# Kernel optimization log

Hardware: AMD Instinct MI355X
Metric: run time of the kernel (lower is better)

Reference implementation:

```python
import jax, jax.numpy as jnp
import numpy as np

B, N, DIM, HEADS, DH = 2, 2048, 512, 8, 64
DIM_INNER = HEADS * DH
SCALE = DH ** -0.5


def setup_inputs() -> dict:
    key = jax.random.key(0)
    ks = jax.random.split(key, 8)
    w = lambda k: jax.random.normal(k, (DIM, DIM_INNER), dtype=jnp.float32) * 0.02
    return {
        'x': jax.random.normal(ks[0], (B, N, DIM), dtype=jnp.float32),
        'w_q_u': w(ks[1]), 'w_k_u': w(ks[2]), 'w_v_u': w(ks[3]),
        'w_q_c': w(ks[4]), 'w_k_c': w(ks[5]), 'w_v_c': w(ks[6]),
        'w_out': jax.random.normal(ks[7], (DIM_INNER, DIM), dtype=jnp.float32) * 0.02,
    }


def _split_heads(t):
    b, n, _ = t.shape
    return t.reshape(b, n, HEADS, DH).transpose(0, 2, 1, 3)  # b h n d


def reference(x, w_q_u, w_k_u, w_v_u, w_q_c, w_k_c, w_v_c, w_out):
    b, n, _ = x.shape
    Qu, Ku, Vu = (_split_heads(x @ w) for w in (w_q_u, w_k_u, w_v_u))
    Qc, Kc, Vc = (_split_heads(x @ w) for w in (w_q_c, w_k_c, w_v_c))

    i = jnp.arange(n)[:, None]
    j = jnp.arange(n)[None, :]
    neg_inf = jnp.float32(-jnp.inf)
    causal_mask = jnp.where(j > i, neg_inf, 0.0)      # -inf strictly above diag
    lookahead_mask = jnp.where(j <= i, neg_inf, 0.0)  # -inf on/below diag
    binary_causal = (j <= i).astype(x.dtype)          # lower-tri ones incl diag

    term1 = jnp.einsum('bhid,bhjd->bhij', Qc, Vu) * SCALE * binary_causal
    sigmoid_term = jax.nn.sigmoid(jnp.einsum('bhid,bhjd->bhij', Qu, Ku) * SCALE + lookahead_mask)
    S_u = jnp.einsum('bhij,bhkj->bhik', term1, sigmoid_term)
    S_c = jnp.einsum('bhid,bhjd->bhij', Qc, Kc) * SCALE + causal_mask

    final_scores = S_c - jax.nn.silu(S_u)
    attn = jax.nn.softmax(final_scores, axis=-1)
    out = jnp.einsum('bhij,bhjd->bhid', attn, Vc)
    out = out.transpose(0, 2, 1, 3).reshape(b, n, DIM_INNER)  # merge heads
    return out @ w_out
```

## Files before the change

kernel.cpp:

```cpp
#include <hip/hip_runtime.h>
#include <hip/hip_bf16.h>

typedef _Float16 h16;
typedef _Float16 h16x8 __attribute__((ext_vector_type(8)));
typedef float f32x4 __attribute__((ext_vector_type(4)));

#define DEVI static __device__ __forceinline__

constexpr int NN = 2048;
constexpr int DIM = 512;
constexpr int NH = 8;
constexpr int DH = 64;
constexpr int BH = 16;
constexpr float FSCALE = 0.125f;

DEVI f32x4 mfma16(h16x8 a, h16x8 b, f32x4 c) {
  return __builtin_amdgcn_mfma_f32_16x16x32_f16(a, b, c, 0, 0, 0);
}

DEVI void glds16(const void* g, void* l) {
  __builtin_amdgcn_global_load_lds(
      (const __attribute__((address_space(1))) unsigned int*)g,
      (__attribute__((address_space(3))) unsigned int*)l, 16, 0, 0);
}

DEVI void tri_decode(int p, int& a, int& b) {
  a = (int)((sqrtf(8.f * p + 1.f) - 1.f) * 0.5f);
  while ((a + 1) * (a + 2) / 2 <= p) ++a;
  while (a * (a + 1) / 2 > p) --a;
  b = p - a * (a + 1) / 2;
}


__global__ __launch_bounds__(256) void k_pack_x(const float* __restrict__ x, h16* __restrict__ xh) {
  int i = (blockIdx.x * 256 + threadIdx.x) * 4;
  float4 v = *(const float4*)(x + i);
  union { h16 h[4]; uint2 u; } pk;
  pk.h[0] = (h16)v.x; pk.h[1] = (h16)v.y; pk.h[2] = (h16)v.z; pk.h[3] = (h16)v.w;
  *(uint2*)(xh + i) = pk.u;
}

struct WPtrs { const float* w[7]; };

__global__ __launch_bounds__(256) void k_pack_w(WPtrs wp, h16* __restrict__ wt) {
  const float* W = wp.w[blockIdx.z];
  h16* out = wt + (size_t)blockIdx.z * DIM * DIM;
  __shared__ h16 t[64][65];
  int k0 = blockIdx.x * 64, o0 = blockIdx.y * 64;
  int c = threadIdx.x & 63, r4 = threadIdx.x >> 6;
#pragma unroll
  for (int rr = 0; rr < 64; rr += 4) {
    int r = rr + r4;
    t[r][c] = (h16)W[(size_t)(k0 + r) * DIM + o0 + c];
  }
  __syncthreads();
#pragma unroll
  for (int rr = 0; rr < 64; rr += 4) {
    int r = rr + r4;
    out[(size_t)(o0 + r) * DIM + k0 + c] = t[c][r];
  }
}

__global__ __launch_bounds__(256) void k_proj(const h16* __restrict__ xh, const h16* __restrict__ wt,
                                              h16* __restrict__ qkv, h16* __restrict__ vcT) {
  __shared__ h16 pool[128 * 136];
  h16* Al = pool;
  h16* Bl = pool + 128 * 64;
  int m0 = blockIdx.x * 128, o0 = blockIdx.y * 128;
  int lane = threadIdx.x & 63, wv = threadIdx.x >> 6;
  int wy = wv >> 1, wx = wv & 1;
  int srow = 32 * wv;
  int lr = lane >> 3, lc = 8 * (lane & 7);
  f32x4 acc[4][4] = {};
  for (int ks0 = 0; ks0 < DIM; ks0 += 64) {
#pragma unroll
    for (int inst = 0; inst < 4; inst++) {
      int r = srow + 8 * inst;
      glds16(xh + (size_t)(m0 + r + lr) * DIM + ks0 + lc, Al + r * 64);
      glds16(wt + (size_t)(o0 + r + lr) * DIM + ks0 + lc, Bl + r * 64);
    }
    __syncthreads();
#pragma unroll
    for (int ks = 0; ks < 2; ks++) {
      h16x8 af[4], bfv[4];
      int co = 32 * ks + 8 * (lane >> 4);
#pragma unroll
      for (int i = 0; i < 4; i++) af[i] = *(const h16x8*)(Al + (64 * wy + 16 * i + (lane & 15)) * 64 + co);
#pragma unroll
      for (int j = 0; j < 4; j++) bfv[j] = *(const h16x8*)(Bl + (64 * wx + 16 * j + (lane & 15)) * 64 + co);
#pragma unroll
      for (int i = 0; i < 4; i++)
#pragma unroll
        for (int j = 0; j < 4; j++) acc[i][j] = mfma16(af[i], bfv[j], acc[i][j]);
    }
    __syncthreads();
  }
  int widx = o0 >> 9;
  float scl = (widx == 0 || widx == 3) ? FSCALE : 1.0f;
  h16 (*Clds)[136] = (h16(*)[136])pool;
#pragma unroll
  for (int i = 0; i < 4; i++)
#pragma unroll
    for (int j = 0; j < 4; j++)
#pragma unroll
      for (int r = 0; r < 4; r++) {
        int rloc = 64 * wy + 16 * i + (lane >> 4) * 4 + r;
        int cloc = 64 * wx + 16 * j + (lane & 15);
        Clds[rloc][cloc] = (h16)(acc[i][j][r] * scl);
      }
  __syncthreads();
  int t = threadIdx.x;
  {
    int rloc = t >> 1, half = t & 1;
    int gi = m0 + rloc;
    int b = gi >> 11, n = gi & 2047;
    int og = o0 + 64 * half;
    int h = (og >> 6) & 7;
    h16* dst = qkv + (((size_t)widx * BH + b * NH + h) * NN + n) * DH;
#pragma unroll
    for (int e = 0; e < 8; e++)
      *(h16x8*)(dst + 8 * e) = *(const h16x8*)&Clds[rloc][64 * half + 8 * e];
  }
  if (widx == 5) {
    int c = t & 127, rq = t >> 7;
    int og = o0 + c;
    int h = (og >> 6) & 7, d = og & 63;
    int b = m0 >> 11, nb = (m0 & 2047) + rq * 64;
    h16* dst = vcT + ((size_t)(b * NH + h) * DH + d) * NN + nb;
#pragma unroll
    for (int g = 0; g < 8; g++) {
      h16x8 w;
#pragma unroll
      for (int e = 0; e < 8; e++) w[e] = Clds[rq * 64 + 8 * g + e][c];
      *(h16x8*)(dst + 8 * g) = w;
    }
  }
}

__global__ __launch_bounds__(256) void k_termsig(const h16* __restrict__ qkv,
                                                 h16* __restrict__ term, h16* __restrict__ sig, int bh0) {
  int pidx = blockIdx.x;
  int lz = blockIdx.z, bh = bh0 + lz;
  int a, bq;
  tri_decode(pidx, a, bq);
  int lane = threadIdx.x & 63, wv = threadIdx.x >> 6;
  int wy = wv >> 1, wx = wv & 1;
  int l15 = lane & 15, q4 = lane >> 4;
  int lr = lane >> 3, lchunk = lane & 7;
  __shared__ h16 pool[128 * 136];
  h16* Al = pool;
  h16* Bl = pool + 128 * 64;
  size_t slot = ((size_t)lz * 136 + (size_t)a * (a + 1) / 2 + bq) * 16384;

  for (int ph = 0; ph < 2; ph++) {
    bool is_sig = (ph == 1);
    int rt = is_sig ? bq : a;
    int jt = is_sig ? a : bq;
    const h16* A  = qkv + ((size_t)(is_sig ? 0 : 3) * BH + bh) * NN * DH;
    const h16* Bv = qkv + ((size_t)(is_sig ? 1 : 2) * BH + bh) * NN * DH;
    h16* out = (is_sig ? sig : term) + slot;
#pragma unroll
    for (int inst = 0; inst < 4; inst++) {
      int rbase = 32 * wv + 8 * inst;
      int row = rbase + lr;
      int sc_ = (lchunk ^ (row & 7)) * 8;
      glds16(A + (size_t)(rt * 128 + row) * DH + sc_, Al + rbase * 64);
      glds16(Bv + (size_t)(jt * 128 + row) * DH + sc_, Bl + rbase * 64);
    }
    __syncthreads();
    f32x4 acc[4][4] = {};
#pragma unroll
    for (int ks = 0; ks < 2; ks++) {
      int co = 32 * ks + 8 * q4;
      h16x8 af[4], bfv[4];
#pragma unroll
      for (int i = 0; i < 4; i++) {
        int row = 64 * wy + 16 * i + l15;
        af[i] = *(const h16x8*)((const char*)Al + ((row * 128 + co * 2) ^ ((row & 7) << 4)));
      }
#pragma unroll
      for (int j = 0; j < 4; j++) {
        int row = 64 * wx + 16 * j + l15;
        bfv[j] = *(const h16x8*)((const char*)Bl + ((row * 128 + co * 2) ^ ((row & 7) << 4)));
      }
#pragma unroll
      for (int i = 0; i < 4; i++)
#pragma unroll
        for (int j = 0; j < 4; j++) acc[i][j] = mfma16(af[i], bfv[j], acc[i][j]);
    }
    __syncthreads();
    h16 (*Clds)[136] = (h16(*)[136])pool;
#pragma unroll
    for (int i = 0; i < 4; i++)
#pragma unroll
      for (int j = 0; j < 4; j++)
#pragma unroll
        for (int r = 0; r < 4; r++) {
          int rloc = 64 * wy + 16 * i + q4 * 4 + r;
          int cloc = 64 * wx + 16 * j + l15;
          int gr = rt * 128 + rloc;
          int gj = jt * 128 + cloc;
          float v = acc[i][j][r];
          float o;
          if (!is_sig) o = (gj <= gr) ? v : 0.f;
          else         o = (gj > gr) ? 1.f / (1.f + __expf(-v)) : 0.f;
          Clds[rloc][cloc] = (h16)o;
        }
    __syncthreads();
    int t = threadIdx.x;
    int rloc = t >> 1, half = t & 1;
    h16* dst = out + (size_t)rloc * 128 + 64 * half;
#pragma unroll
    for (int e = 0; e < 8; e++)
      *(h16x8*)(dst + 8 * e) = *(const h16x8*)&Clds[rloc][64 * half + 8 * e];
    __syncthreads();
  }
}

__global__ __launch_bounds__(256) void k_scores(const h16* __restrict__ qkv,
                                                const h16* __restrict__ term, const h16* __restrict__ sig,
                                                const h16* __restrict__ vcT,
                                                h16* __restrict__ Ot,
                                                float* __restrict__ psum, int bh0) {
  __shared__ h16 pool[128 * 136];
  h16* Al = pool;
  h16* Bl = pool + 128 * 64;
  int nwg = gridDim.x;
  int q = nwg >> 3, rmd = nwg & 7;
  int xcd = blockIdx.x & 7, idx = blockIdx.x >> 3;
  int wg = (xcd < rmd) ? xcd * (q + 1) + idx : rmd * (q + 1) + (xcd - rmd) * q + idx;
  int lz = wg / 136, r = wg % 136;
  int It = 15, base = 0;
  while (r - base >= It + 1) { base += It + 1; --It; }
  int Kt = r - base;
  int bh = bh0 + lz;
  int i0 = It * 128, k0 = Kt * 128;
  int triIt = It * (It + 1) / 2;
  const h16* termP = term + (size_t)lz * 136 * 16384;
  const h16* sigP  = sig + (size_t)lz * 136 * 16384;
  int lane = threadIdx.x & 63, wv = threadIdx.x >> 6;
  int wy = wv >> 1, wx = wv & 1;
  int l15 = lane & 15, q4 = lane >> 4;
  int lr = lane >> 3, lchunk = lane & 7;
  f32x4 acc[4][4] = {};
  for (int js = k0; js < i0 + 128; js += 64) {
    int jt = js >> 7, joff = js & 64;
    const h16* At = termP + (size_t)(triIt + jt) * 16384;
    const h16* Bt = sigP + (size_t)(jt * (jt + 1) / 2 + Kt) * 16384;
#pragma unroll
    for (int inst = 0; inst < 4; inst++) {
      int rbase = 32 * wv + 8 * inst;
      int row = rbase + lr;
      int sc_ = (lchunk ^ (row & 7)) * 8;
      glds16(At + (size_t)row * 128 + joff + sc_, Al + rbase * 64);
      glds16(Bt + (size_t)row * 128 + joff + sc_, Bl + rbase * 64);
    }
    __syncthreads();
#pragma unroll
    for (int ks = 0; ks < 2; ks++) {
      int co = 32 * ks + 8 * q4;
      h16x8 af[4], bfv[4];
#pragma unroll
      for (int i = 0; i < 4; i++) {
        int row = 64 * wy + 16 * i + l15;
        af[i] = *(const h16x8*)((const char*)Al + ((row * 128 + co * 2) ^ ((row & 7) << 4)));
      }
#pragma unroll
      for (int j = 0; j < 4; j++) {
        int row = 64 * wx + 16 * j + l15;
        bfv[j] = *(const h16x8*)((const char*)Bl + ((row * 128 + co * 2) ^ ((row & 7) << 4)));
      }
#pragma unroll
      for (int i = 0; i < 4; i++)
#pragma unroll
        for (int j = 0; j < 4; j++) acc[i][j] = mfma16(af[i], bfv[j], acc[i][j]);
    }
    __syncthreads();
  }
#pragma unroll
  for (int i = 0; i < 4; i++)
#pragma unroll
    for (int j = 0; j < 4; j++)
#pragma unroll
      for (int rr = 0; rr < 4; rr++) {
        float xv = acc[i][j][rr];
        acc[i][j][rr] = -xv / (1.f + __expf(-xv));
      }
  const h16* Q  = qkv + ((size_t)3 * BH + bh) * NN * DH;
  const h16* Kc = qkv + ((size_t)4 * BH + bh) * NN * DH;
#pragma unroll
  for (int d2 = 0; d2 < 2; d2++) {
    int kb = 32 * d2 + 8 * q4;
    h16x8 af[4], bfv[4];
#pragma unroll
    for (int i = 0; i < 4; i++)
      af[i] = *(const h16x8*)(Q + (size_t)(i0 + 64 * wy + 16 * i + l15) * DH + kb);
#pragma unroll
    for (int j = 0; j < 4; j++)
      bfv[j] = *(const h16x8*)(Kc + (size_t)(k0 + 64 * wx + 16 * j + l15) * DH + kb);
#pragma unroll
    for (int i = 0; i < 4; i++)
#pragma unroll
      for (int j = 0; j < 4; j++) acc[i][j] = mfma16(af[i], bfv[j], acc[i][j]);
  }
  h16 (*Clds)[136] = (h16(*)[136])pool;
#pragma unroll
  for (int i = 0; i < 4; i++)
#pragma unroll
    for (int j = 0; j < 4; j++)
#pragma unroll
      for (int rr = 0; rr < 4; rr++) {
        int rloc = 64 * wy + 16 * i + q4 * 4 + rr;
        int cloc = 64 * wx + 16 * j + l15;
        float pv = (k0 + cloc <= i0 + rloc) ? __expf(acc[i][j][rr]) : 0.f;
        Clds[rloc][cloc] = (h16)pv;
      }
  __syncthreads();
  int t = threadIdx.x;
  {
    int rloc = t >> 1, half = t & 1;
    float ls = 0.f;
#pragma unroll
    for (int e = 0; e < 8; e++) {
      h16x8 v8 = *(const h16x8*)&Clds[rloc][64 * half + 8 * e];
#pragma unroll
      for (int qe = 0; qe < 8; qe++) ls += (float)v8[qe];
    }
    ls += __shfl_xor(ls, 1);
    if (half == 0) psum[((size_t)lz * 16 + Kt) * NN + i0 + rloc] = ls;
  }
  const h16* VT = vcT + (size_t)bh * DH * NN;
  f32x4 acc2[4][2] = {};
#pragma unroll
  for (int ks = 0; ks < 4; ks++) {
    int co = 32 * ks + 8 * q4;
    h16x8 bf2[2];
#pragma unroll
    for (int n = 0; n < 2; n++)
      bf2[n] = *(const h16x8*)(VT + (size_t)(32 * wx + 16 * n + l15) * NN + k0 + co);
#pragma unroll
    for (int m = 0; m < 4; m++) {
      h16x8 af2 = *(const h16x8*)&Clds[64 * wy + 16 * m + l15][co];
#pragma unroll
      for (int n = 0; n < 2; n++) acc2[m][n] = mfma16(af2, bf2[n], acc2[m][n]);
    }
  }
  h16* ob = Ot + ((size_t)lz * 136 + triIt + Kt) * (128 * 64);
#pragma unroll
  for (int m = 0; m < 4; m++)
#pragma unroll
    for (int n = 0; n < 2; n++)
#pragma unroll
      for (int rr = 0; rr < 4; rr++) {
        int row = 64 * wy + 16 * m + 4 * q4 + rr;
        int col = 32 * wx + 16 * n + l15;
        ob[row * 64 + col] = (h16)acc2[m][n][rr];
      }
}

__global__ __launch_bounds__(256) void k_pvm(const h16* __restrict__ Ot,
                                             const float* __restrict__ psum,
                                             h16* __restrict__ attn, int bh0) {
  int It = blockIdx.x, lz = blockIdx.y, bh = bh0 + lz;
  int t = threadIdx.x;
  int rloc = t >> 1, dh = (t & 1) * 32;
  int i = It * 128 + rloc;
  int ntk = It + 1;
  int triIt = It * (It + 1) / 2;
  const float* pl = psum + (size_t)lz * 16 * NN + i;
  float L = 0.f;
  for (int k = 0; k < ntk; k++) L += pl[(size_t)k * NN];
  float invL = 1.f / L;
  float acc[32] = {};
  for (int k = 0; k < ntk; k++) {
    const h16* ob = Ot + ((size_t)lz * 136 + triIt + k) * (128 * 64) + (size_t)rloc * 64 + dh;
#pragma unroll
    for (int e = 0; e < 4; e++) {
      h16x8 v = *(const h16x8*)(ob + 8 * e);
#pragma unroll
      for (int qe = 0; qe < 8; qe++) acc[8 * e + qe] += (float)v[qe];
    }
  }
  int hh = bh & 7, b = bh >> 3;
  h16* dst = attn + ((size_t)b * NN + i) * DIM + hh * DH + dh;
#pragma unroll
  for (int g = 0; g < 4; g++) {
    h16x8 o;
#pragma unroll
    for (int qe = 0; qe < 8; qe++) o[qe] = (h16)(acc[g * 8 + qe] * invL);
    *(h16x8*)(dst + 8 * g) = o;
  }
}

__global__ __launch_bounds__(256) void k_outproj(const h16* __restrict__ attn, const h16* __restrict__ Wt,
                                                 float* __restrict__ out) {
  int m0 = blockIdx.x * 64, o0 = blockIdx.y * 64;
  int lane = threadIdx.x & 63, wv = threadIdx.x >> 6;
  int kb = 8 * (lane >> 4);
  f32x4 acc[4] = {};
  const h16* ap = attn + (size_t)(m0 + 16 * wv + (lane & 15)) * DIM + kb;
  const h16* bp = Wt + (size_t)(o0 + (lane & 15)) * DIM + kb;
  for (int k0 = 0; k0 < DIM; k0 += 32) {
    h16x8 af = *(const h16x8*)(ap + k0);
#pragma unroll
    for (int t = 0; t < 4; t++) {
      h16x8 bfv = *(const h16x8*)(bp + (size_t)(16 * t) * DIM + k0);
      acc[t] = mfma16(af, bfv, acc[t]);
    }
  }
  int ri = m0 + 16 * wv + (lane >> 4) * 4;
  int c0 = o0 + (lane & 15);
#pragma unroll
  for (int t = 0; t < 4; t++)
#pragma unroll
    for (int r = 0; r < 4; r++) out[(size_t)(ri + r) * DIM + c0 + 16 * t] = acc[t][r];
}


extern "C" void kernel_launch(void* const* d_in, const int* in_sizes, int n_in,
                              void* d_out, int out_size, void* d_ws, size_t ws_size,
                              hipStream_t stream) {
  const float* x = (const float*)d_in[0];
  WPtrs wp;
  for (int i = 0; i < 7; i++) wp.w[i] = (const float*)d_in[1 + i];

  char* p = (char*)d_ws;
  auto alloc = [&](size_t bytes) {
    void* r = (void*)p;
    p += (bytes + 255) & ~(size_t)255;
    return r;
  };
  h16* xh   = (h16*)alloc((size_t)4096 * DIM * 2);
  h16* wt   = (h16*)alloc((size_t)7 * DIM * DIM * 2);
  h16* qkv  = (h16*)alloc((size_t)6 * BH * NN * DH * 2);
  h16* vcT  = (h16*)alloc((size_t)BH * DH * NN * 2);
  h16* attn = (h16*)alloc((size_t)4096 * DIM * 2);
  size_t used = (size_t)(p - (char*)d_ws);
  size_t ts_bh = (size_t)136 * 16384 * 2;
  size_t ot_bh = (size_t)136 * 128 * 64 * 2;
  size_t pp_bh = (size_t)16 * NN * 4;
  size_t avail = ws_size > used ? ws_size - used : 0;
  int CH = 16;
  while (CH > 1 && (size_t)CH * (ts_bh * 2 + ot_bh + pp_bh) > avail) CH >>= 1;
  h16* term   = (h16*)alloc((size_t)CH * ts_bh);
  h16* sig    = (h16*)alloc((size_t)CH * ts_bh);
  h16* Ot     = (h16*)alloc((size_t)CH * ot_bh);
  float* psum = (float*)alloc((size_t)CH * pp_bh);

  k_pack_x<<<dim3(2048), dim3(256), 0, stream>>>(x, xh);
  k_pack_w<<<dim3(8, 8, 7), dim3(256), 0, stream>>>(wp, wt);
  k_proj<<<dim3(32, 24), dim3(256), 0, stream>>>(xh, wt, qkv, vcT);

  for (int c0 = 0; c0 < BH; c0 += CH) {
    k_termsig<<<dim3(136, 1, CH), dim3(256), 0, stream>>>(qkv, term, sig, c0);
    k_scores<<<dim3(136 * CH), dim3(256), 0, stream>>>(qkv, term, sig, vcT, Ot, psum, c0);
    k_pvm<<<dim3(16, CH), dim3(256), 0, stream>>>(Ot, psum, attn, c0);
  }

  k_outproj<<<dim3(64, 8), dim3(256), 0, stream>>>(attn, wt + (size_t)6 * DIM * DIM, (float*)d_out);
}
```

Baseline: 260.2 us.

## Fuse partial-output reduction and normalization with output projection; specialize diagonal masking

Adds a kernel that reduces the per-tile partial attention outputs, normalizes them by the summed row denominators, and multiplies by the output projection weights in one pass. This removes the intermediate attn buffer write/read and one launch when all heads fit in a single chunk. The fused kernel uses only 256 blocks of 16 rows, so parallelism is lower and each block reloads the full weight matrix from global memory. Separately, the exp/mask store in the score kernel is split so that off-diagonal tiles skip the causal comparison.

Result: faster. 254.0 us (-2.4%).

```diff
diff --git a/kernel.cpp b/kernel.cpp
--- a/kernel.cpp
+++ b/kernel.cpp
@@ -304,17 +304,30 @@
       for (int j = 0; j < 4; j++) acc[i][j] = mfma16(af[i], bfv[j], acc[i][j]);
   }
   h16 (*Clds)[136] = (h16(*)[136])pool;
-#pragma unroll
-  for (int i = 0; i < 4; i++)
-#pragma unroll
-    for (int j = 0; j < 4; j++)
-#pragma unroll
-      for (int rr = 0; rr < 4; rr++) {
-        int rloc = 64 * wy + 16 * i + q4 * 4 + rr;
-        int cloc = 64 * wx + 16 * j + l15;
-        float pv = (k0 + cloc <= i0 + rloc) ? __expf(acc[i][j][rr]) : 0.f;
-        Clds[rloc][cloc] = (h16)pv;
-      }
+  if (It == Kt) {
+#pragma unroll
+    for (int i = 0; i < 4; i++)
+#pragma unroll
+      for (int j = 0; j < 4; j++)
+#pragma unroll
+        for (int rr = 0; rr < 4; rr++) {
+          int rloc = 64 * wy + 16 * i + q4 * 4 + rr;
+          int cloc = 64 * wx + 16 * j + l15;
+          float pv = (cloc <= rloc) ? __expf(acc[i][j][rr]) : 0.f;
+          Clds[rloc][cloc] = (h16)pv;
+        }
+  } else {
+#pragma unroll
+    for (int i = 0; i < 4; i++)
+#pragma unroll
+      for (int j = 0; j < 4; j++)
+#pragma unroll
+        for (int rr = 0; rr < 4; rr++) {
+          int rloc = 64 * wy + 16 * i + q4 * 4 + rr;
+          int cloc = 64 * wx + 16 * j + l15;
+          Clds[rloc][cloc] = (h16)__expf(acc[i][j][rr]);
+        }
+  }
   __syncthreads();
   int t = threadIdx.x;
   {
@@ -356,6 +369,70 @@
         int col = 32 * wx + 16 * n + l15;
         ob[row * 64 + col] = (h16)acc2[m][n][rr];
       }
+}
+
+__global__ __launch_bounds__(256) void k_pvout(const h16* __restrict__ Ot,
+                                               const float* __restrict__ psum,
+                                               const h16* __restrict__ Wt,
+                                               float* __restrict__ out) {
+  int m0 = blockIdx.x * 16;
+  int b = m0 >> 11;
+  int i0 = m0 & 2047;
+  int It = i0 >> 7;
+  int ntk = It + 1, triIt = It * (It + 1) / 2;
+  int rbase = i0 & 127;
+  __shared__ h16 attnL[16][520];
+  int t = threadIdx.x;
+  {
+    int r = t >> 4, cseg = t & 15;
+    int col0 = cseg * 32;
+    int h = col0 >> 6;
+    int bh = b * 8 + h;
+    int coff = col0 & 63;
+    const float* pl = psum + (size_t)bh * 16 * NN + i0 + r;
+    float L = 0.f;
+    for (int k = 0; k < ntk; k++) L += pl[(size_t)k * NN];
+    float invL = 1.f / L;
+    float acc[32] = {};
+    const h16* obase = Ot + ((size_t)bh * 136 + triIt) * 8192 + (size_t)(rbase + r) * 64 + coff;
+    for (int k = 0; k < ntk; k++) {
+      const h16* ob = obase + (size_t)k * 8192;
+#pragma unroll
+      for (int e = 0; e < 4; e++) {
+        h16x8 v = *(const h16x8*)(ob + 8 * e);
+#pragma unroll
+        for (int qe = 0; qe < 8; qe++) acc[8 * e + qe] += (float)v[qe];
+      }
+    }
+#pragma unroll
+    for (int e = 0; e < 4; e++) {
+      h16x8 o;
+#pragma unroll
+      for (int qe = 0; qe < 8; qe++) o[qe] = (h16)(acc[8 * e + qe] * invL);
+      *(h16x8*)&attnL[r][col0 + 8 * e] = o;
+    }
+  }
+  __syncthreads();
+  int lane = t & 63, wv = t >> 6;
+  int l15 = lane & 15, q4 = lane >> 4;
+  f32x4 acc2[2][4] = {};
+  for (int k0 = 0; k0 < DIM; k0 += 32) {
+    h16x8 af = *(const h16x8*)&attnL[l15][k0 + 8 * q4];
+#pragma unroll
+    for (int c = 0; c < 2; c++)
+#pragma unroll
+      for (int tt = 0; tt < 4; tt++) {
+        h16x8 bf = *(const h16x8*)(Wt + (size_t)(wv * 128 + c * 64 + tt * 16 + l15) * DIM + k0 + 8 * q4);
+        acc2[c][tt] = mfma16(af, bf, acc2[c][tt]);
+      }
+  }
+#pragma unroll
+  for (int c = 0; c < 2; c++)
+#pragma unroll
+    for (int tt = 0; tt < 4; tt++)
+#pragma unroll
+      for (int rr = 0; rr < 4; rr++)
+        out[(size_t)(m0 + 4 * q4 + rr) * DIM + wv * 128 + c * 64 + tt * 16 + l15] = acc2[c][tt][rr];
 }
 
 __global__ __launch_bounds__(256) void k_pvm(const h16* __restrict__ Ot,
@@ -446,16 +523,22 @@
   h16* sig    = (h16*)alloc((size_t)CH * ts_bh);
   h16* Ot     = (h16*)alloc((size_t)CH * ot_bh);
   float* psum = (float*)alloc((size_t)CH * pp_bh);
+  const h16* wout = wt + (size_t)6 * DIM * DIM;
 
   k_pack_x<<<dim3(2048), dim3(256), 0, stream>>>(x, xh);
   k_pack_w<<<dim3(8, 8, 7), dim3(256), 0, stream>>>(wp, wt);
   k_proj<<<dim3(32, 24), dim3(256), 0, stream>>>(xh, wt, qkv, vcT);
 
-  for (int c0 = 0; c0 < BH; c0 += CH) {
-    k_termsig<<<dim3(136, 1, CH), dim3(256), 0, stream>>>(qkv, term, sig, c0);
-    k_scores<<<dim3(136 * CH), dim3(256), 0, stream>>>(qkv, term, sig, vcT, Ot, psum, c0);
-    k_pvm<<<dim3(16, CH), dim3(256), 0, stream>>>(Ot, psum, attn, c0);
-  }
-
-  k_outproj<<<dim3(64, 8), dim3(256), 0, stream>>>(attn, wt + (size_t)6 * DIM * DIM, (float*)d_out);
-}
+  if (CH == 16) {
+    k_termsig<<<dim3(136, 1, 16), dim3(256), 0, stream>>>(qkv, term, sig, 0);
+    k_scores<<<dim3(136 * 16), dim3(256), 0, stream>>>(qkv, term, sig, vcT, Ot, psum, 0);
+    k_pvout<<<dim3(256), dim3(256), 0, stream>>>(Ot, psum, wout, (float*)d_out);
+  } else {
+    for (int c0 = 0; c0 < BH; c0 += CH) {
+      k_termsig<<<dim3(136, 1, CH), dim3(256), 0, stream>>>(qkv, term, sig, c0);
+      k_scores<<<dim3(136 * CH), dim3(256), 0, stream>>>(qkv, term, sig, vcT, Ot, psum, c0);
+      k_pvm<<<dim3(16, CH), dim3(256), 0, stream>>>(Ot, psum, attn, c0);
+    }
+    k_outproj<<<dim3(64, 8), dim3(256), 0, stream>>>(attn, wout, (float*)d_out);
+  }
+}
```
